# Kernel optimization log

Hardware: AMD Instinct MI355X
Metric: run time of the kernel (lower is better)

## Reference

```python
import jax, jax.numpy as jnp
import numpy as np

N_NODES = 50000


def _gcn_conv(x, edge_index, W, b, num_nodes):
    """PyG GCNConv: h = D^{-1/2} (A + I) D^{-1/2} (x W) + b."""
    # add self loops
    loops = jnp.arange(num_nodes, dtype=edge_index.dtype)
    src = jnp.concatenate([edge_index[0], loops])  # [E + N]
    dst = jnp.concatenate([edge_index[1], loops])
    # symmetric degree normalization (edge weight 1.0, incl. self loops)
    deg = jax.ops.segment_sum(jnp.ones_like(src, dtype=x.dtype), dst,
                              num_segments=num_nodes)
    dinv = jnp.where(deg > 0, jax.lax.rsqrt(deg), 0.0)
    norm = dinv[src] * dinv[dst]  # [E + N]
    h = x @ W  # [N, H] dense GEMM first (PyG applies lin before propagate)
    msgs = h[src] * norm[:, None]  # gather + scale, [E + N, H]
    out = jax.ops.segment_sum(msgs, dst, num_segments=num_nodes)  # scatter-add
    return out + b


def setup_inputs() -> dict:
    key = jax.random.key(0)
    ks = jax.random.split(key, 6)
    F_in, H = 100, 1024
    state = jax.random.normal(ks[0], (N_NODES, F_in, 1), dtype=jnp.float32)
    edge_index = jax.random.randint(ks[1], (2, 200000), 0, N_NODES, dtype=jnp.int64)
    W1 = jax.random.normal(ks[2], (F_in, H), dtype=jnp.float32) / np.sqrt(F_in)
    b1 = jax.random.normal(ks[3], (H,), dtype=jnp.float32) * 0.01
    W_head = jax.random.normal(ks[4], (H, 1), dtype=jnp.float32) / np.sqrt(H)
    b_head = jax.random.normal(ks[5], (1,), dtype=jnp.float32) * 0.01
    return {"state": state, "edge_index": edge_index, "W1": W1, "b1": b1,
            "W_head": W_head, "b_head": b_head}


def reference(state, edge_index, W1, b1, W_head, b_head):
    x = state.reshape(state.shape[0], state.shape[1])  # (N, F, 1) -> (N, F)
    h = _gcn_conv(x, edge_index, W1, b1, N_NODES)      # GCNConv 100 -> 1024
    return h @ W_head + b_head                          # linear head -> (N, 1)
```

## Files before the change

kernel.cpp:

```cpp
#include <hip/hip_runtime.h>


#define N_NODES 50000
#define F_IN    100
#define H_DIM   1024
#define N_EDGES 200000

__global__ void k_fold_deg(const float* __restrict__ W1, const float* __restrict__ b1,
                           const float* __restrict__ Wh, const float* __restrict__ bh,
                           const int* __restrict__ dst,
                           float* __restrict__ w, float* __restrict__ c,
                           unsigned* __restrict__ deg)
{
    const int b = blockIdx.x;
    const int t = threadIdx.x;
    if (b <= 100) {
        const float* row = (b < 100) ? (W1 + (size_t)b * H_DIM) : b1;
        float s = 0.0f;
        for (int h = t; h < H_DIM; h += 256) s += row[h] * Wh[h];
        #pragma unroll
        for (int off = 32; off > 0; off >>= 1) s += __shfl_down(s, off, 64);
        __shared__ float red[4];
        const int wave = t >> 6, lane = t & 63;
        if (lane == 0) red[wave] = s;
        __syncthreads();
        if (t == 0) {
            float tot = red[0] + red[1] + red[2] + red[3];
            if (b < 100) w[b] = tot;
            else         *c  = tot + bh[0];
        }
    } else {
        const int e = (b - 101) * 256 + t;
        if (e < N_EDGES) atomicAdd(&deg[dst[e]], 1u);
    }
}

__global__ void k_score(const float* __restrict__ x, const float* __restrict__ w,
                        const unsigned* __restrict__ deg, float* __restrict__ u)
{
    const int gwave = (blockIdx.x * blockDim.x + threadIdx.x) >> 6;
    const int lane  = threadIdx.x & 63;
    if (gwave >= N_NODES) return;
    const float* row = x + (size_t)gwave * F_IN;
    float s = row[lane] * w[lane];
    if (lane < F_IN - 64) s += row[64 + lane] * w[64 + lane];
    #pragma unroll
    for (int off = 32; off > 0; off >>= 1) s += __shfl_down(s, off, 64);
    if (lane == 0) u[gwave] = s * rsqrtf((float)deg[gwave] + 1.0f);
}

__global__ void k_scatter(const int* __restrict__ src, const int* __restrict__ dst,
                          const float* __restrict__ u, float* __restrict__ acc)
{
    const int e = blockIdx.x * blockDim.x + threadIdx.x;
    if (e < N_EDGES) unsafeAtomicAdd(&acc[dst[e]], u[src[e]]);
}

__global__ void k_final(const unsigned* __restrict__ deg, const float* __restrict__ u,
                        const float* __restrict__ acc, const float* __restrict__ c,
                        float* __restrict__ out)
{
    const int i = blockIdx.x * blockDim.x + threadIdx.x;
    if (i < N_NODES)
        out[i] = rsqrtf((float)deg[i] + 1.0f) * (acc[i] + u[i]) + c[0];
}

extern "C" void kernel_launch(void* const* d_in, const int* in_sizes, int n_in,
                              void* d_out, int out_size, void* d_ws, size_t ws_size,
                              hipStream_t stream)
{
    const float* x   = (const float*)d_in[0];
    const int*   ei  = (const int*)  d_in[1];
    const float* W1  = (const float*)d_in[2];
    const float* b1  = (const float*)d_in[3];
    const float* Wh  = (const float*)d_in[4];
    const float* bh  = (const float*)d_in[5];
    float*       out = (float*)d_out;

    const int* src = ei;
    const int* dst = ei + N_EDGES;

    float*    ws_f = (float*)d_ws;
    float*    w    = ws_f;
    float*    c    = ws_f + 100;
    unsigned* deg  = (unsigned*)(ws_f + 128);
    float*    acc  = ws_f + 128 + N_NODES;
    float*    u    = ws_f + 128 + 2 * N_NODES;

    hipMemsetAsync(deg, 0, 2 * N_NODES * sizeof(float), stream);

    k_fold_deg<<<101 + (N_EDGES + 255) / 256, 256, 0, stream>>>(
        W1, b1, Wh, bh, dst, w, c, deg);
    k_score<<<(N_NODES + 3) / 4, 256, 0, stream>>>(x, w, deg, u);
    k_scatter<<<(N_EDGES + 255) / 256, 256, 0, stream>>>(src, dst, u, acc);
    k_final<<<(N_NODES + 255) / 256, 256, 0, stream>>>(deg, u, acc, c, out);
}
```

Before: 108.8 us.

## Fuse all GCN stages into one cooperative persistent kernel with grid syncs

Replaces the memset plus four kernel launches with a single cooperative kernel of 512 blocks that zeroes buffers, folds W1·Wh, counts degrees, computes per-node scores, scatters and finalizes, separated by grid-wide barriers. The aim is to remove per-launch overhead and the separate memset. Degree normalization moves from the score phase into the scatter and final phases, so the degree counting can share a phase with the score computation. In exchange it adds three grid.sync barriers and fixes parallelism at 512 blocks, so each stage is handled by grid-stride loops rather than a full-size grid.

Result: slower. 276.1 us (+153.9%).

```diff
diff --git a/kernel.cpp b/kernel.cpp
--- a/kernel.cpp
+++ b/kernel.cpp
@@ -1,68 +1,80 @@
 #include <hip/hip_runtime.h>
+#include <hip/hip_cooperative_groups.h>
+
+namespace cg = cooperative_groups;
 
 
 #define N_NODES 50000
 #define F_IN    100
 #define H_DIM   1024
 #define N_EDGES 200000
+#define GRID    512
+#define BLK     256
 
-__global__ void k_fold_deg(const float* __restrict__ W1, const float* __restrict__ b1,
-                           const float* __restrict__ Wh, const float* __restrict__ bh,
-                           const int* __restrict__ dst,
-                           float* __restrict__ w, float* __restrict__ c,
-                           unsigned* __restrict__ deg)
+__global__ void __launch_bounds__(BLK)
+k_gcn_all(const float* __restrict__ x,   const int* __restrict__ ei,
+          const float* __restrict__ W1,  const float* __restrict__ b1,
+          const float* __restrict__ Wh,  const float* __restrict__ bh,
+          float* __restrict__ out,
+          float* __restrict__ wbuf, float* __restrict__ cbuf,
+          unsigned* __restrict__ deg, float* __restrict__ acc,
+          float* __restrict__ sbuf)
 {
-    const int b = blockIdx.x;
-    const int t = threadIdx.x;
-    if (b <= 100) {
-        const float* row = (b < 100) ? (W1 + (size_t)b * H_DIM) : b1;
-        float s = 0.0f;
-        for (int h = t; h < H_DIM; h += 256) s += row[h] * Wh[h];
+    cg::grid_group grid = cg::this_grid();
+    const int tid   = blockIdx.x * BLK + threadIdx.x;
+    const int nthr  = GRID * BLK;
+    const int gwave = tid >> 6;
+    const int lane  = tid & 63;
+    const int nwave = nthr >> 6;
+    const int* src  = ei;
+    const int* dst  = ei + N_EDGES;
+
+    {
+        unsigned* z = deg;
+        for (int i = tid; i < 2 * N_NODES; i += nthr) z[i] = 0u;
+        if (gwave <= 100) {
+            const float* row = (gwave < 100) ? (W1 + (size_t)gwave * H_DIM) : b1;
+            float s = 0.0f;
+            #pragma unroll
+            for (int k = 0; k < H_DIM / 64; ++k) {
+                const int h = lane + 64 * k;
+                s += row[h] * Wh[h];
+            }
+            #pragma unroll
+            for (int off = 32; off > 0; off >>= 1) s += __shfl_down(s, off, 64);
+            if (lane == 0) {
+                if (gwave < 100) wbuf[gwave] = s;
+                else             cbuf[0]     = s + bh[0];
+            }
+        }
+    }
+    grid.sync();
+
+    for (int e = tid; e < N_EDGES; e += nthr)
+        atomicAdd(&deg[dst[e]], 1u);
+
+    for (int i = gwave; i < N_NODES; i += nwave) {
+        const float* row = x + (size_t)i * F_IN;
+        float s = row[lane] * wbuf[lane];
+        if (lane < F_IN - 64) s += row[64 + lane] * wbuf[64 + lane];
         #pragma unroll
         for (int off = 32; off > 0; off >>= 1) s += __shfl_down(s, off, 64);
-        __shared__ float red[4];
-        const int wave = t >> 6, lane = t & 63;
-        if (lane == 0) red[wave] = s;
-        __syncthreads();
-        if (t == 0) {
-            float tot = red[0] + red[1] + red[2] + red[3];
-            if (b < 100) w[b] = tot;
-            else         *c  = tot + bh[0];
-        }
-    } else {
-        const int e = (b - 101) * 256 + t;
-        if (e < N_EDGES) atomicAdd(&deg[dst[e]], 1u);
+        if (lane == 0) sbuf[i] = s;
     }
-}
+    grid.sync();
 
-__global__ void k_score(const float* __restrict__ x, const float* __restrict__ w,
-                        const unsigned* __restrict__ deg, float* __restrict__ u)
-{
-    const int gwave = (blockIdx.x * blockDim.x + threadIdx.x) >> 6;
-    const int lane  = threadIdx.x & 63;
-    if (gwave >= N_NODES) return;
-    const float* row = x + (size_t)gwave * F_IN;
-    float s = row[lane] * w[lane];
-    if (lane < F_IN - 64) s += row[64 + lane] * w[64 + lane];
-    #pragma unroll
-    for (int off = 32; off > 0; off >>= 1) s += __shfl_down(s, off, 64);
-    if (lane == 0) u[gwave] = s * rsqrtf((float)deg[gwave] + 1.0f);
-}
+    for (int e = tid; e < N_EDGES; e += nthr) {
+        const int sn = src[e], dn = dst[e];
+        const float us = sbuf[sn] * rsqrtf((float)deg[sn] + 1.0f);
+        unsafeAtomicAdd(&acc[dn], us);
+    }
+    grid.sync();
 
-__global__ void k_scatter(const int* __restrict__ src, const int* __restrict__ dst,
-                          const float* __restrict__ u, float* __restrict__ acc)
-{
-    const int e = blockIdx.x * blockDim.x + threadIdx.x;
-    if (e < N_EDGES) unsafeAtomicAdd(&acc[dst[e]], u[src[e]]);
-}
-
-__global__ void k_final(const unsigned* __restrict__ deg, const float* __restrict__ u,
-                        const float* __restrict__ acc, const float* __restrict__ c,
-                        float* __restrict__ out)
-{
-    const int i = blockIdx.x * blockDim.x + threadIdx.x;
-    if (i < N_NODES)
-        out[i] = rsqrtf((float)deg[i] + 1.0f) * (acc[i] + u[i]) + c[0];
+    const float cv = cbuf[0];
+    for (int i = tid; i < N_NODES; i += nthr) {
+        const float dv = rsqrtf((float)deg[i] + 1.0f);
+        out[i] = dv * acc[i] + dv * dv * sbuf[i] + cv;
+    }
 }
 
 extern "C" void kernel_launch(void* const* d_in, const int* in_sizes, int n_in,
@@ -77,21 +89,17 @@
     const float* bh  = (const float*)d_in[5];
     float*       out = (float*)d_out;
 
-    const int* src = ei;
-    const int* dst = ei + N_EDGES;
-
     float*    ws_f = (float*)d_ws;
-    float*    w    = ws_f;
-    float*    c    = ws_f + 100;
+    float*    wbuf = ws_f;
+    float*    cbuf = ws_f + 100;
     unsigned* deg  = (unsigned*)(ws_f + 128);
     float*    acc  = ws_f + 128 + N_NODES;
-    float*    u    = ws_f + 128 + 2 * N_NODES;
+    float*    sbuf = ws_f + 128 + 2 * N_NODES;
 
-    hipMemsetAsync(deg, 0, 2 * N_NODES * sizeof(float), stream);
-
-    k_fold_deg<<<101 + (N_EDGES + 255) / 256, 256, 0, stream>>>(
-        W1, b1, Wh, bh, dst, w, c, deg);
-    k_score<<<(N_NODES + 3) / 4, 256, 0, stream>>>(x, w, deg, u);
-    k_scatter<<<(N_EDGES + 255) / 256, 256, 0, stream>>>(src, dst, u, acc);
-    k_final<<<(N_NODES + 255) / 256, 256, 0, stream>>>(deg, u, acc, c, out);
+    void* args[] = { (void*)&x,   (void*)&ei,   (void*)&W1, (void*)&b1,
+                     (void*)&Wh,  (void*)&bh,   (void*)&out,
+                     (void*)&wbuf,(void*)&cbuf, (void*)&deg,
+                     (void*)&acc, (void*)&sbuf };
+    hipLaunchCooperativeKernel((const void*)k_gcn_all, dim3(GRID), dim3(BLK),
+                               args, 0, stream);
 }
```

## Fuse memset into fold kernel, merge degree count with scoring, vectorize scatter/final

Applied to the files above, without the earlier changes.

Replaces the hipMemsetAsync with float4 zeroing inside the weight-fold kernel and moves the degree atomics into the score kernel. The degree normalization of the source node is now applied at scatter time, so scoring no longer has to wait for degrees. Scatter handles two edges per thread with int2 loads, and the final kernel uses float4/uint4 vector loads. This removes one launch and one memset from the four-kernel pipeline, at the cost of extra deg gathers and rsqrt work in the scatter kernel.

New measurement: 103.5 us. 4.8% less time.

```diff
diff --git a/kernel.cpp b/kernel.cpp
--- a/kernel.cpp
+++ b/kernel.cpp
@@ -6,18 +6,22 @@
 #define H_DIM   1024
 #define N_EDGES 200000
 
-__global__ void k_fold_deg(const float* __restrict__ W1, const float* __restrict__ b1,
-                           const float* __restrict__ Wh, const float* __restrict__ bh,
-                           const int* __restrict__ dst,
-                           float* __restrict__ w, float* __restrict__ c,
-                           unsigned* __restrict__ deg)
+__global__ void __launch_bounds__(256)
+k0_zero_fold(const float* __restrict__ W1, const float* __restrict__ b1,
+             const float* __restrict__ Wh, const float* __restrict__ bh,
+             float* __restrict__ w, float* __restrict__ c,
+             float4* __restrict__ zero_region)
 {
     const int b = blockIdx.x;
     const int t = threadIdx.x;
     if (b <= 100) {
         const float* row = (b < 100) ? (W1 + (size_t)b * H_DIM) : b1;
         float s = 0.0f;
-        for (int h = t; h < H_DIM; h += 256) s += row[h] * Wh[h];
+        #pragma unroll
+        for (int k = 0; k < H_DIM / 256; ++k) {
+            const int h = t + 256 * k;
+            s += row[h] * Wh[h];
+        }
         #pragma unroll
         for (int off = 32; off > 0; off >>= 1) s += __shfl_down(s, off, 64);
         __shared__ float red[4];
@@ -25,44 +29,76 @@
         if (lane == 0) red[wave] = s;
         __syncthreads();
         if (t == 0) {
-            float tot = red[0] + red[1] + red[2] + red[3];
+            const float tot = red[0] + red[1] + red[2] + red[3];
             if (b < 100) w[b] = tot;
             else         *c  = tot + bh[0];
         }
     } else {
-        const int e = (b - 101) * 256 + t;
-        if (e < N_EDGES) atomicAdd(&deg[dst[e]], 1u);
+        const int g = (b - 101) * 256 + t;
+        if (g < (2 * N_NODES) / 4)
+            zero_region[g] = make_float4(0.f, 0.f, 0.f, 0.f);
     }
 }
 
-__global__ void k_score(const float* __restrict__ x, const float* __restrict__ w,
-                        const unsigned* __restrict__ deg, float* __restrict__ u)
+__global__ void __launch_bounds__(256)
+k1_deg_score(const float* __restrict__ x, const int* __restrict__ ei,
+             const float* __restrict__ w,
+             unsigned* __restrict__ deg, float* __restrict__ sbuf)
 {
-    const int gwave = (blockIdx.x * blockDim.x + threadIdx.x) >> 6;
-    const int lane  = threadIdx.x & 63;
-    if (gwave >= N_NODES) return;
-    const float* row = x + (size_t)gwave * F_IN;
-    float s = row[lane] * w[lane];
-    if (lane < F_IN - 64) s += row[64 + lane] * w[64 + lane];
-    #pragma unroll
-    for (int off = 32; off > 0; off >>= 1) s += __shfl_down(s, off, 64);
-    if (lane == 0) u[gwave] = s * rsqrtf((float)deg[gwave] + 1.0f);
+    const int tid   = blockIdx.x * 256 + threadIdx.x;
+    const int gwave = tid >> 6;
+    const int lane  = tid & 63;
+
+    if (tid < N_EDGES / 4) {
+        const int4 d4 = ((const int4*)(ei + N_EDGES))[tid];
+        atomicAdd(&deg[d4.x], 1u);
+        atomicAdd(&deg[d4.y], 1u);
+        atomicAdd(&deg[d4.z], 1u);
+        atomicAdd(&deg[d4.w], 1u);
+    }
+
+    if (gwave < N_NODES) {
+        const float* row = x + (size_t)gwave * F_IN;
+        float s = row[lane] * w[lane];
+        if (lane < F_IN - 64) s += row[64 + lane] * w[64 + lane];
+        #pragma unroll
+        for (int off = 32; off > 0; off >>= 1) s += __shfl_down(s, off, 64);
+        if (lane == 0) sbuf[gwave] = s;
+    }
 }
 
-__global__ void k_scatter(const int* __restrict__ src, const int* __restrict__ dst,
-                          const float* __restrict__ u, float* __restrict__ acc)
+__global__ void __launch_bounds__(256)
+k2_scatter(const int* __restrict__ ei, const unsigned* __restrict__ deg,
+           const float* __restrict__ sbuf, float* __restrict__ acc)
 {
-    const int e = blockIdx.x * blockDim.x + threadIdx.x;
-    if (e < N_EDGES) unsafeAtomicAdd(&acc[dst[e]], u[src[e]]);
+    const int g = blockIdx.x * 256 + threadIdx.x;
+    if (g >= N_EDGES / 2) return;
+    const int2 s2 = ((const int2*)ei)[g];
+    const int2 d2 = ((const int2*)(ei + N_EDGES))[g];
+    const float u0 = sbuf[s2.x] * rsqrtf((float)deg[s2.x] + 1.0f);
+    const float u1 = sbuf[s2.y] * rsqrtf((float)deg[s2.y] + 1.0f);
+    unsafeAtomicAdd(&acc[d2.x], u0);
+    unsafeAtomicAdd(&acc[d2.y], u1);
 }
 
-__global__ void k_final(const unsigned* __restrict__ deg, const float* __restrict__ u,
-                        const float* __restrict__ acc, const float* __restrict__ c,
-                        float* __restrict__ out)
+__global__ void __launch_bounds__(256)
+k3_final(const uint4* __restrict__ deg4, const float4* __restrict__ acc4,
+         const float4* __restrict__ s4, const float* __restrict__ c,
+         float4* __restrict__ out4)
 {
-    const int i = blockIdx.x * blockDim.x + threadIdx.x;
-    if (i < N_NODES)
-        out[i] = rsqrtf((float)deg[i] + 1.0f) * (acc[i] + u[i]) + c[0];
+    const int g = blockIdx.x * 256 + threadIdx.x;
+    if (g >= N_NODES / 4) return;
+    const uint4  d = deg4[g];
+    const float4 a = acc4[g];
+    const float4 s = s4[g];
+    const float  cv = c[0];
+    float4 o;
+    float dv;
+    dv  = rsqrtf((float)d.x + 1.0f); o.x = dv * a.x + dv * dv * s.x + cv;
+    dv  = rsqrtf((float)d.y + 1.0f); o.y = dv * a.y + dv * dv * s.y + cv;
+    dv  = rsqrtf((float)d.z + 1.0f); o.z = dv * a.z + dv * dv * s.z + cv;
+    dv  = rsqrtf((float)d.w + 1.0f); o.w = dv * a.w + dv * dv * s.w + cv;
+    out4[g] = o;
 }
 
 extern "C" void kernel_launch(void* const* d_in, const int* in_sizes, int n_in,
@@ -77,21 +113,16 @@
     const float* bh  = (const float*)d_in[5];
     float*       out = (float*)d_out;
 
-    const int* src = ei;
-    const int* dst = ei + N_EDGES;
-
     float*    ws_f = (float*)d_ws;
     float*    w    = ws_f;
     float*    c    = ws_f + 100;
     unsigned* deg  = (unsigned*)(ws_f + 128);
     float*    acc  = ws_f + 128 + N_NODES;
-    float*    u    = ws_f + 128 + 2 * N_NODES;
+    float*    sbuf = ws_f + 128 + 2 * N_NODES;
 
-    hipMemsetAsync(deg, 0, 2 * N_NODES * sizeof(float), stream);
-
-    k_fold_deg<<<101 + (N_EDGES + 255) / 256, 256, 0, stream>>>(
-        W1, b1, Wh, bh, dst, w, c, deg);
-    k_score<<<(N_NODES + 3) / 4, 256, 0, stream>>>(x, w, deg, u);
-    k_scatter<<<(N_EDGES + 255) / 256, 256, 0, stream>>>(src, dst, u, acc);
-    k_final<<<(N_NODES + 255) / 256, 256, 0, stream>>>(deg, u, acc, c, out);
+    k0_zero_fold<<<199, 256, 0, stream>>>(W1, b1, Wh, bh, w, c, (float4*)deg);
+    k1_deg_score<<<(N_NODES * 64 + 255) / 256, 256, 0, stream>>>(x, ei, w, deg, sbuf);
+    k2_scatter<<<(N_EDGES / 2 + 255) / 256, 256, 0, stream>>>(ei, deg, sbuf, acc);
+    k3_final<<<(N_NODES / 4 + 255) / 256, 256, 0, stream>>>(
+        (const uint4*)deg, (const float4*)acc, (const float4*)sbuf, c, (float4*)out);
 }
```
